# Optimization experiments

Hardware: AMD Instinct MI355X
Metric: run time of the kernel (lower is better)

The kernel has to match this reference:

```python
import jax, jax.numpy as jnp
import numpy as np

T = 2048          # num tokens (single long prefill sequence)
HID = 2048        # hidden_size
NH = 16           # num query heads
NKV = 2           # num kv heads
HD = 128          # head_dim (kv_channels)
ROPE_BASE = 10000.0


def setup_inputs() -> dict:
    key = jax.random.key(0)
    k1, k2, k3, k4, k5 = jax.random.split(key, 5)
    s = 0.02
    return {
        "hidden_states": jax.random.normal(k1, (T, HID), dtype=jnp.float32),
        "positions": jnp.arange(T, dtype=jnp.int64 if jax.config.jax_enable_x64 else jnp.int32),
        "Wq": jax.random.normal(k2, (NH * HD, HID), dtype=jnp.float32) * s,
        "Wk": jax.random.normal(k3, (NKV * HD, HID), dtype=jnp.float32) * s,
        "Wv": jax.random.normal(k4, (NKV * HD, HID), dtype=jnp.float32) * s,
        "Wo": jax.random.normal(k5, (HID, NH * HD), dtype=jnp.float32) * s,
    }


def _rope_cos_sin(positions):
    # fp32 RoPE tables, HF-style (concat of freqs with itself)
    inv_freq = 1.0 / (ROPE_BASE ** (jnp.arange(0, HD, 2, dtype=jnp.float32) / HD))
    freqs = positions.astype(jnp.float32)[:, None] * inv_freq[None, :]   # [T, HD/2]
    emb = jnp.concatenate([freqs, freqs], axis=-1)                        # [T, HD]
    return jnp.cos(emb)[:, None, :], jnp.sin(emb)[:, None, :]             # [T,1,HD]


def _rotate_half(x):
    x1, x2 = jnp.split(x, 2, axis=-1)
    return jnp.concatenate([-x2, x1], axis=-1)


def reference(hidden_states, positions, Wq, Wk, Wv, Wo):
    dtype = hidden_states.dtype
    # fused QKV projection (weights concatenated once, single GEMM)
    W_fused = jnp.concatenate([Wq, Wk, Wv], axis=0)            # [q+2kv, HID]
    qkv = hidden_states @ W_fused.T                             # [T, q+2kv]
    q, k, v = jnp.split(qkv, [NH * HD, NH * HD + NKV * HD], axis=-1)

    # fp32 RoPE on q/k
    cos, sin = _rope_cos_sin(positions)                         # [T,1,HD]
    qf = q.reshape(T, NH, HD).astype(jnp.float32)
    kf = k.reshape(T, NKV, HD).astype(jnp.float32)
    qf = qf * cos + _rotate_half(qf) * sin
    kf = kf * cos + _rotate_half(kf) * sin
    q = qf.astype(dtype)                                        # [T,NH,HD]
    k = kf.astype(dtype)                                        # [T,NKV,HD]
    v = v.reshape(T, NKV, HD)

    # causal GQA attention (same math as the paged-attention kernel on one seq)
    group = NH // NKV
    k_rep = jnp.repeat(k, group, axis=1)                        # [T,NH,HD]
    v_rep = jnp.repeat(v, group, axis=1)                        # [T,NH,HD]
    scale = HD ** -0.5
    scores = jnp.einsum('qhd,khd->hqk', q, k_rep) * scale       # [NH,T,T]
    causal = jnp.tril(jnp.ones((T, T), dtype=bool))
    scores = jnp.where(causal[None], scores, jnp.finfo(scores.dtype).min)
    probs = jax.nn.softmax(scores, axis=-1)
    attn = jnp.einsum('hqk,khd->qhd', probs, v_rep).reshape(T, NH * HD)

    return attn @ Wo.T                                          # [T, HID]
```

## Files before the change

### kernel.cpp

```cpp
#include <hip/hip_runtime.h>

#define T_TOK 2048
#define HID   2048
#define NH    16
#define NKV   2
#define HD    128
#define QDIM  (NH * HD)
#define KVDIM (NKV * HD)
#define QKVDIM (QDIM + 2 * KVDIM)

typedef float          f32x4  __attribute__((ext_vector_type(4)));
typedef unsigned short u16x8  __attribute__((ext_vector_type(8)));
typedef __bf16         bf16x8 __attribute__((ext_vector_type(8)));

__device__ __forceinline__ unsigned short f2bf(float f) {
    __bf16 h = (__bf16)f;
    return __builtin_bit_cast(unsigned short, h);
}
__device__ __forceinline__ float bf2f(unsigned short u) {
    return (float)__builtin_bit_cast(__bf16, u);
}

__device__ __forceinline__ f32x4 mfma16(u16x8 a, u16x8 b, f32x4 c) {
    return __builtin_amdgcn_mfma_f32_16x16x32_bf16(
        __builtin_bit_cast(bf16x8, a), __builtin_bit_cast(bf16x8, b), c, 0, 0, 0);
}

#define QSCL 0.12751743f
#define DEFER_THR 11.5416f

__global__ __launch_bounds__(256) void pack_bf16_all(
    const float* __restrict__ hidden, const float* __restrict__ Wq,
    const float* __restrict__ Wk, const float* __restrict__ Wv,
    const float* __restrict__ Wo,
    unsigned short* __restrict__ hb, unsigned short* __restrict__ Wf,
    unsigned short* __restrict__ Wob)
{
    const int b = blockIdx.x;
    const float* src; unsigned short* dst; size_t off;
    if      (b < 2048) { src = hidden; dst = hb;            off = (size_t)b * 2048; }
    else if (b < 4096) { src = Wq;     dst = Wf;            off = (size_t)(b - 2048) * 2048; }
    else if (b < 4352) { src = Wk;     dst = Wf + 4194304;  off = (size_t)(b - 4096) * 2048; }
    else if (b < 4608) { src = Wv;     dst = Wf + 4718592;  off = (size_t)(b - 4352) * 2048; }
    else               { src = Wo;     dst = Wob;           off = (size_t)(b - 4608) * 2048; }

    const size_t i = off + threadIdx.x * 8;
    float4 f0 = *reinterpret_cast<const float4*>(src + i);
    float4 f1 = *reinterpret_cast<const float4*>(src + i + 4);
    u16x8 o;
    o[0]=f2bf(f0.x); o[1]=f2bf(f0.y); o[2]=f2bf(f0.z); o[3]=f2bf(f0.w);
    o[4]=f2bf(f1.x); o[5]=f2bf(f1.y); o[6]=f2bf(f1.z); o[7]=f2bf(f1.w);
    *reinterpret_cast<u16x8*>(dst + i) = o;
}

template<bool BF16OUT>
__global__ __launch_bounds__(256) void gemm_bf16(
    const unsigned short* __restrict__ A,
    const unsigned short* __restrict__ B,
    void* __restrict__ Cv,
    int K, int NC, int nbx)
{
    __shared__ alignas(16) unsigned short As[2][128 * 64];
    __shared__ alignas(16) unsigned short Bs[2][128 * 64];

    const int tid  = threadIdx.x;
    const int lane = tid & 63;
    const int w    = tid >> 6;
    const int lg   = lane >> 4, lc = lane & 15;

    const int cpx = gridDim.x >> 3;
    const int wg  = (blockIdx.x & 7) * cpx + (blockIdx.x >> 3);
    const int m0  = (wg / nbx) * 128, n0 = (wg % nbx) * 128;

    const int rowL = lane >> 3;
    const int gS   = (lane & 7) ^ rowL;
    const int wr   = (w >> 1) * 64, wc = (w & 1) * 64;

    f32x4 acc[4][4] = {};

    auto stage = [&](int buf, int kb) {
        #pragma unroll
        for (int ci = 0; ci < 4; ci++) {
            const int chunk = w * 4 + ci;
            const int row   = chunk * 8 + rowL;
            const unsigned short* gpA = &A[(size_t)(m0 + row) * K + kb + gS * 8];
            __builtin_amdgcn_global_load_lds(
                (const __attribute__((address_space(1))) void*)gpA,
                (__attribute__((address_space(3))) void*)(&As[buf][chunk * 512]),
                16, 0, 0);
            const unsigned short* gpB = &B[(size_t)(n0 + row) * K + kb + gS * 8];
            __builtin_amdgcn_global_load_lds(
                (const __attribute__((address_space(1))) void*)gpB,
                (__attribute__((address_space(3))) void*)(&Bs[buf][chunk * 512]),
                16, 0, 0);
        }
    };

    stage(0, 0);
    const int nk = K >> 6;
    for (int t = 0; t < nk; ++t) {
        if (t + 1 < nk) {
            stage((t + 1) & 1, (t + 1) * 64);
            asm volatile("s_waitcnt vmcnt(8)" ::: "memory");
        } else {
            asm volatile("s_waitcnt vmcnt(0)" ::: "memory");
        }
        __syncthreads();

        const unsigned short* As_ = As[t & 1];
        const unsigned short* Bs_ = Bs[t & 1];
        #pragma unroll
        for (int kk = 0; kk < 2; kk++) {
            u16x8 af[4], bf[4];
            #pragma unroll
            for (int mi = 0; mi < 4; mi++) {
                const int r = wr + mi * 16 + lc;
                const int g = (kk * 4 + lg) ^ (lc & 7);
                af[mi] = *reinterpret_cast<const u16x8*>(&As_[r * 64 + g * 8]);
            }
            #pragma unroll
            for (int ni = 0; ni < 4; ni++) {
                const int r = wc + ni * 16 + lc;
                const int g = (kk * 4 + lg) ^ (lc & 7);
                bf[ni] = *reinterpret_cast<const u16x8*>(&Bs_[r * 64 + g * 8]);
            }
            #pragma unroll
            for (int mi = 0; mi < 4; mi++)
                #pragma unroll
                for (int ni = 0; ni < 4; ni++)
                    acc[mi][ni] = mfma16(af[mi], bf[ni], acc[mi][ni]);
        }
        __syncthreads();
    }

    #pragma unroll
    for (int mi = 0; mi < 4; mi++)
        #pragma unroll
        for (int ni = 0; ni < 4; ni++)
            #pragma unroll
            for (int j = 0; j < 4; j++) {
                const size_t idx = (size_t)(m0 + wr + mi * 16 + lg * 4 + j) * NC
                                   + n0 + wc + ni * 16 + lc;
                if constexpr (BF16OUT)
                    ((unsigned short*)Cv)[idx] = f2bf(acc[mi][ni][j]);
                else
                    ((float*)Cv)[idx] = acc[mi][ni][j];
            }
}

__global__ __launch_bounds__(256) void rope_kernel(
    const unsigned short* __restrict__ qkvb,
    const int* __restrict__ positions,
    unsigned short* __restrict__ qr,
    unsigned short* __restrict__ kr)
{
    const int t   = blockIdx.x;
    const int tid = threadIdx.x;
    __shared__ float cosv[64], sinv[64];

    if (tid < 64) {
        float invf = expf(-(float)tid * 0.14391156831212787f);
        float f = (float)positions[t] * invf;
        cosv[tid] = cosf(f);
        sinv[tid] = sinf(f);
    }
    __syncthreads();

    const unsigned short* row = qkvb + (size_t)t * QKVDIM;

    for (int i = tid; i < NH * 64; i += 256) {
        int hh = i >> 6, j = i & 63;
        float x1 = bf2f(row[hh * HD + j]);
        float x2 = bf2f(row[hh * HD + j + 64]);
        float c = cosv[j], s = sinv[j];
        qr[(size_t)t * QDIM + hh * HD + j]      = f2bf((x1 * c - x2 * s) * QSCL);
        qr[(size_t)t * QDIM + hh * HD + j + 64] = f2bf((x2 * c + x1 * s) * QSCL);
    }
    if (tid < NKV * 64) {
        int hh = tid >> 6, j = tid & 63;
        float x1 = bf2f(row[QDIM + hh * HD + j]);
        float x2 = bf2f(row[QDIM + hh * HD + j + 64]);
        float c = cosv[j], s = sinv[j];
        kr[(size_t)t * KVDIM + hh * HD + j]      = f2bf(x1 * c - x2 * s);
        kr[(size_t)t * KVDIM + hh * HD + j + 64] = f2bf(x2 * c + x1 * s);
    }
}

__global__ __launch_bounds__(256) void v_transpose(
    const unsigned short* __restrict__ qkvb,
    unsigned short* __restrict__ vt)
{
    __shared__ unsigned short tile[64][72];
    const int tid = threadIdx.x;
    const int t0  = blockIdx.x * 64;
    const int d0  = blockIdx.y * 64;

    {
        int r = tid >> 2;
        int c = (tid & 3) * 16;
        const unsigned short* src =
            &qkvb[(size_t)(t0 + r) * QKVDIM + QDIM + KVDIM + d0 + c];
        *reinterpret_cast<u16x8*>(&tile[r][c])     = *reinterpret_cast<const u16x8*>(src);
        *reinterpret_cast<u16x8*>(&tile[r][c + 8]) = *reinterpret_cast<const u16x8*>(src + 8);
    }
    __syncthreads();
    {
        int dr = tid >> 3;
        int tc = (tid & 7) * 8;
        #pragma unroll
        for (int i = 0; i < 2; i++) {
            int d = dr + i * 32;
            u16x8 ov;
            #pragma unroll
            for (int e = 0; e < 8; e++) ov[e] = tile[tc + e][d];
            *reinterpret_cast<u16x8*>(&vt[(size_t)(d0 + d) * T_TOK + t0 + tc]) = ov;
        }
    }
}

__global__ __launch_bounds__(256) void attn_kernel(
    const unsigned short* __restrict__ q,
    const unsigned short* __restrict__ k,
    const unsigned short* __restrict__ vt,
    unsigned short* __restrict__ o,
    float* __restrict__ pO,
    float* __restrict__ pML)
{
    __shared__ alignas(16) unsigned short Ks[2][64 * 128];
    __shared__ alignas(16) unsigned short Vs[2][128 * 64];
    __shared__ alignas(16) unsigned short P[4][16][72];

    const int tid  = threadIdx.x;
    const int lane = tid & 63;
    const int w    = tid >> 6;
    const int lg   = lane >> 4, lc = lane & 15;
    const int b    = blockIdx.x;
    const int h    = b & 15;
    const int idx  = b >> 4;

    int tau, c0;
    if (idx <= 16)      { tau = 15 + idx; c0 = 0; }
    else if (idx == 17) { tau = 31;       c0 = 1; }
    else {
        int j = idx - 18, kk = 15 - (j >> 1);
        if ((j & 1) == 0) { tau = kk - 1;  c0 = 0; }
        else              { tau = kk + 15; c0 = 1; }
    }
    const int kstart = c0 << 4;
    const int kcnt   = min(16, tau + 1 - kstart);

    const int q0   = tau * 64 + w * 16;
    const int hk   = h >> 3;
    const int xr   = (lc & 7) << 4;

    const int krow_l = (lane >> 4);
    const int kgS    = (lane & 15);
    const int vrow_l = (lane >> 3);
    const int vgS    = (lane & 7);

    u16x8 qf[4];
    #pragma unroll
    for (int dc = 0; dc < 4; dc++)
        qf[dc] = *reinterpret_cast<const u16x8*>(
            &q[(size_t)(q0 + lc) * QDIM + h * HD + dc * 32 + lg * 8]);

    float mrow = -1e30f, ell = 0.f;
    f32x4 oacc[8] = {};

    auto stage = [&](int buf, int kb) {
        #pragma unroll
        for (int ci = 0; ci < 4; ci++) {
            const int chunk = w * 4 + ci;
            const int row   = chunk * 4 + krow_l;
            const int gSk   = kgS ^ (row & 7);
            const unsigned short* gp =
                &k[(size_t)(kb + row) * KVDIM + hk * HD + gSk * 8];
            __builtin_amdgcn_global_load_lds(
                (const __attribute__((address_space(1))) void*)gp,
                (__attribute__((address_space(3))) void*)(&Ks[buf][chunk * 512]),
                16, 0, 0);
        }
        #pragma unroll
        for (int ci = 0; ci < 4; ci++) {
            const int chunk = w * 4 + ci;
            const int dr    = chunk * 8 + vrow_l;
            const int gSv   = vgS ^ (dr & 7);
            const unsigned short* gp =
                &vt[(size_t)(hk * HD + dr) * T_TOK + kb + gSv * 8];
            __builtin_amdgcn_global_load_lds(
                (const __attribute__((address_space(1))) void*)gp,
                (__attribute__((address_space(3))) void*)(&Vs[buf][chunk * 512]),
                16, 0, 0);
        }
    };

    stage(0, kstart * 64);
    for (int it = 0; it < kcnt; ++it) {
        if (it + 1 < kcnt) {
            stage((it + 1) & 1, (kstart + it + 1) * 64);
            asm volatile("s_waitcnt vmcnt(8)" ::: "memory");
        } else {
            asm volatile("s_waitcnt vmcnt(0)" ::: "memory");
        }
        __syncthreads();

        const int kb = (kstart + it) * 64;
        const char* KsB = (const char*)Ks[it & 1];
        const char* VsB = (const char*)Vs[it & 1];

        float sc[4][4];
        const bool dia = (kb + 63 > q0);
        #pragma unroll
        for (int c4 = 0; c4 < 4; c4++) {
            const int row = c4 * 16 + lc;
            f32x4 s = {0.f, 0.f, 0.f, 0.f};
            #pragma unroll
            for (int dc = 0; dc < 4; dc++) {
                u16x8 kf = *reinterpret_cast<const u16x8*>(
                    KsB + row * 256 + ((dc * 64 + lg * 16) ^ xr));
                s = mfma16(kf, qf[dc], s);
            }
            if (dia) {
                #pragma unroll
                for (int j = 0; j < 4; j++) {
                    const int kpos = kb + c4 * 16 + lg * 4 + j;
                    sc[c4][j] = (kpos <= q0 + lc) ? s[j] : -1e30f;
                }
            } else {
                #pragma unroll
                for (int j = 0; j < 4; j++) sc[c4][j] = s[j];
            }
        }

        float t01 = fmaxf(fmaxf(sc[0][0], sc[0][1]), fmaxf(sc[0][2], sc[0][3]));
        float t23 = fmaxf(fmaxf(sc[1][0], sc[1][1]), fmaxf(sc[1][2], sc[1][3]));
        float t45 = fmaxf(fmaxf(sc[2][0], sc[2][1]), fmaxf(sc[2][2], sc[2][3]));
        float t67 = fmaxf(fmaxf(sc[3][0], sc[3][1]), fmaxf(sc[3][2], sc[3][3]));
        float tmx = fmaxf(fmaxf(t01, t23), fmaxf(t45, t67));
        tmx = fmaxf(tmx, __shfl_xor(tmx, 16));
        tmx = fmaxf(tmx, __shfl_xor(tmx, 32));

        float mn;
        if (__all(tmx <= mrow + DEFER_THR)) {
            mn = mrow;
        } else {
            mn = fmaxf(mrow, tmx);
            float alpha = __builtin_amdgcn_exp2f(mrow - mn);
            mrow = mn;
            ell *= alpha;
            float aj[4];
            #pragma unroll
            for (int j = 0; j < 4; j++)
                aj[j] = __shfl(alpha, lg * 4 + j);
            #pragma unroll
            for (int d8 = 0; d8 < 8; d8++)
                #pragma unroll
                for (int j = 0; j < 4; j++)
                    oacc[d8][j] *= aj[j];
        }

        float rs = 0.f;
        #pragma unroll
        for (int c4 = 0; c4 < 4; c4++) {
            float p0 = __builtin_amdgcn_exp2f(sc[c4][0] - mn);
            float p1 = __builtin_amdgcn_exp2f(sc[c4][1] - mn);
            float p2 = __builtin_amdgcn_exp2f(sc[c4][2] - mn);
            float p3 = __builtin_amdgcn_exp2f(sc[c4][3] - mn);
            rs += (p0 + p1) + (p2 + p3);
            ushort4 pk;
            pk.x = f2bf(p0); pk.y = f2bf(p1); pk.z = f2bf(p2); pk.w = f2bf(p3);
            *reinterpret_cast<ushort4*>(&P[w][lc][c4 * 16 + lg * 4]) = pk;
        }
        rs += __shfl_xor(rs, 16);
        rs += __shfl_xor(rs, 32);
        ell += rs;

        asm volatile("s_waitcnt lgkmcnt(0)" ::: "memory");
        __builtin_amdgcn_sched_barrier(0);

        u16x8 pf0 = *reinterpret_cast<const u16x8*>(&P[w][lc][lg * 8]);
        u16x8 pf1 = *reinterpret_cast<const u16x8*>(&P[w][lc][32 + lg * 8]);

        #pragma unroll
        for (int d8 = 0; d8 < 8; d8++) {
            const int drow = d8 * 16 + lc;
            u16x8 vf0 = *reinterpret_cast<const u16x8*>(
                VsB + drow * 128 + ((lg * 16) ^ xr));
            u16x8 vf1 = *reinterpret_cast<const u16x8*>(
                VsB + drow * 128 + ((lg * 16 + 64) ^ xr));
            oacc[d8] = mfma16(pf0, vf0, oacc[d8]);
            oacc[d8] = mfma16(pf1, vf1, oacc[d8]);
        }
        __syncthreads();
    }

    if (tau < 16) {
        float ej[4];
        #pragma unroll
        for (int j = 0; j < 4; j++)
            ej[j] = __shfl(ell, lg * 4 + j);
        #pragma unroll
        for (int d8 = 0; d8 < 8; d8++)
            #pragma unroll
            for (int j = 0; j < 4; j++) {
                float val = oacc[d8][j] / ej[j];
                o[(size_t)(q0 + lg * 4 + j) * QDIM + h * HD + d8 * 16 + lc] = f2bf(val);
            }
    } else {
        const int s = (h * 16 + (tau - 16)) * 2 + c0;
        float* po = pO + (size_t)s * 8192;
        #pragma unroll
        for (int d8 = 0; d8 < 8; d8++)
            #pragma unroll
            for (int j = 0; j < 4; j++)
                po[(w * 16 + lg * 4 + j) * 128 + d8 * 16 + lc] = oacc[d8][j];
        if (lg == 0) {
            pML[s * 128 + w * 16 + lc]      = mrow;
            pML[s * 128 + 64 + w * 16 + lc] = ell;
        }
    }
}

__global__ __launch_bounds__(256) void attn_combine(
    const float* __restrict__ pO,
    const float* __restrict__ pML,
    unsigned short* __restrict__ o)
{
    const int b  = blockIdx.x;
    const int h  = b >> 4, ti = b & 15;
    const int tau = 16 + ti;
    const int s0 = (h * 16 + ti) * 2, s1 = s0 + 1;

    const int tid = threadIdx.x;
    const int r   = tid >> 2;
    const int cg  = (tid & 3) * 32;

    const float m1 = pML[s0 * 128 + r],      m2 = pML[s1 * 128 + r];
    const float l1 = pML[s0 * 128 + 64 + r], l2 = pML[s1 * 128 + 64 + r];
    const float M  = fmaxf(m1, m2);
    const float w1 = __builtin_amdgcn_exp2f(m1 - M);
    const float w2 = __builtin_amdgcn_exp2f(m2 - M);
    const float rn = 1.0f / (w1 * l1 + w2 * l2);

    const float* o1 = pO + (size_t)s0 * 8192 + r * 128 + cg;
    const float* o2 = pO + (size_t)s1 * 8192 + r * 128 + cg;
    unsigned short* dst = o + (size_t)(tau * 64 + r) * QDIM + h * HD + cg;

    #pragma unroll
    for (int i = 0; i < 8; i++) {
        float4 a = *reinterpret_cast<const float4*>(o1 + i * 4);
        float4 c = *reinterpret_cast<const float4*>(o2 + i * 4);
        ushort4 pk;
        pk.x = f2bf((w1 * a.x + w2 * c.x) * rn);
        pk.y = f2bf((w1 * a.y + w2 * c.y) * rn);
        pk.z = f2bf((w1 * a.z + w2 * c.z) * rn);
        pk.w = f2bf((w1 * a.w + w2 * c.w) * rn);
        *reinterpret_cast<ushort4*>(dst + i * 4) = pk;
    }
}

extern "C" void kernel_launch(void* const* d_in, const int* in_sizes, int n_in,
                              void* d_out, int out_size, void* d_ws, size_t ws_size,
                              hipStream_t stream) {
    const float* hidden    = (const float*)d_in[0];
    const int*   positions = (const int*)d_in[1];
    const float* Wq        = (const float*)d_in[2];
    const float* Wk        = (const float*)d_in[3];
    const float* Wv        = (const float*)d_in[4];
    const float* Wo        = (const float*)d_in[5];
    float*       out       = (float*)d_out;

    char* ws = (char*)d_ws;
    unsigned short* qkvb = (unsigned short*)(ws);
    unsigned short* qr  = (unsigned short*)(ws + 20971520);
    unsigned short* kr  = (unsigned short*)(ws + 29360128);
    unsigned short* vt  = (unsigned short*)(ws + 30408704);
    unsigned short* att = (unsigned short*)(ws + 31457280);
    unsigned short* hb  = (unsigned short*)(ws + 39845888);
    unsigned short* Wf  = (unsigned short*)(ws + 48234496);
    unsigned short* Wob = (unsigned short*)(ws + 58720256);
    float* pO  = (float*)(ws);
    float* pML = (float*)(ws + 16777216);

    pack_bf16_all<<<6656, 256, 0, stream>>>(hidden, Wq, Wk, Wv, Wo, hb, Wf, Wob);
    gemm_bf16<true><<<320, 256, 0, stream>>>(hb, Wf, qkvb, HID, QKVDIM, QKVDIM / 128);
    rope_kernel<<<T_TOK, 256, 0, stream>>>(qkvb, positions, qr, kr);
    v_transpose<<<dim3(T_TOK / 64, KVDIM / 64), 256, 0, stream>>>(qkvb, vt);
    attn_kernel<<<NH * 48, 256, 0, stream>>>(qr, kr, vt, att, pO, pML);
    attn_combine<<<256, 256, 0, stream>>>(pO, pML, att);
    gemm_bf16<false><<<256, 256, 0, stream>>>(att, Wob, out, QDIM, HID, HID / 128);
}
```

Measured before the change: 145.6 us.

## Split attention into 8-tile KV chunks with table schedule, fuse rope and V transpose

Attention work is now split into chunks of at most 8 KV tiles, so long query tiles get up to 4 partial blocks. The blocks are ordered by a static schedule table, 1280 blocks instead of 768, with a combine kernel that merges up to 4 partials. The double-buffered K/V staging is replaced by single-buffered LDS, which halves shared memory per block and should let more blocks reside on each CU. The RoPE and V-transpose kernels are merged into one launch to save a kernel launch. In exchange, loads no longer overlap compute within a block, and the extra partial writes and combine reads add memory traffic.

```diff
diff --git a/kernel.cpp b/kernel.cpp
--- a/kernel.cpp
+++ b/kernel.cpp
@@ -28,6 +28,29 @@
 
 #define QSCL 0.12751743f
 #define DEFER_THR 11.5416f
+
+__device__ __forceinline__ float* slotO(char* b, int s) {
+    return (float*)(s < 640 ? b + (size_t)s * 32768
+                            : b + 39845888 + (size_t)(s - 640) * 32768);
+}
+#define PML_OFF 56623104
+
+__device__ const unsigned char SCH_TAU[80] = {
+ 31,31,31,31, 30,30,30, 29,29,29, 28,28,28, 27,27,27, 26,26,26, 25,25,25, 24,24,24, 23,23,23,
+ 22,22, 21,21, 20,20, 19,19, 18,18, 17,17, 16,16, 15,15,
+ 14,13,12,11,10,9,8,7,
+ 30,22,14,6, 29,21,13,5, 28,20,12,4, 27,19,11,3, 26,18,10,2, 25,17,9,1, 24,16,8,0 };
+__device__ const unsigned char SCH_C[80] = {
+ 0,1,2,3, 0,1,2, 0,1,2, 0,1,2, 0,1,2, 0,1,2, 0,1,2, 0,1,2, 0,1,2,
+ 0,1, 0,1, 0,1, 0,1, 0,1, 0,1, 0,1, 0,1,
+ 0,0,0,0,0,0,0,0,
+ 3,2,1,0, 3,2,1,0, 3,2,1,0, 3,2,1,0, 3,2,1,0, 3,2,1,0, 3,2,1,0 };
+
+__device__ __forceinline__ int tile_local(int tau) {
+    return tau < 16 ? (tau - 8) * 2
+         : tau < 24 ? 16 + (tau - 16) * 3
+                    : 40 + (tau - 24) * 4;
+}
 
 __global__ __launch_bounds__(256) void pack_bf16_all(
     const float* __restrict__ hidden, const float* __restrict__ Wq,
@@ -148,72 +171,68 @@
             }
 }
 
-__global__ __launch_bounds__(256) void rope_kernel(
+__global__ __launch_bounds__(256) void rope_vt(
     const unsigned short* __restrict__ qkvb,
     const int* __restrict__ positions,
     unsigned short* __restrict__ qr,
-    unsigned short* __restrict__ kr)
-{
-    const int t   = blockIdx.x;
-    const int tid = threadIdx.x;
-    __shared__ float cosv[64], sinv[64];
-
-    if (tid < 64) {
-        float invf = expf(-(float)tid * 0.14391156831212787f);
-        float f = (float)positions[t] * invf;
-        cosv[tid] = cosf(f);
-        sinv[tid] = sinf(f);
-    }
-    __syncthreads();
-
-    const unsigned short* row = qkvb + (size_t)t * QKVDIM;
-
-    for (int i = tid; i < NH * 64; i += 256) {
-        int hh = i >> 6, j = i & 63;
-        float x1 = bf2f(row[hh * HD + j]);
-        float x2 = bf2f(row[hh * HD + j + 64]);
-        float c = cosv[j], s = sinv[j];
-        qr[(size_t)t * QDIM + hh * HD + j]      = f2bf((x1 * c - x2 * s) * QSCL);
-        qr[(size_t)t * QDIM + hh * HD + j + 64] = f2bf((x2 * c + x1 * s) * QSCL);
-    }
-    if (tid < NKV * 64) {
-        int hh = tid >> 6, j = tid & 63;
-        float x1 = bf2f(row[QDIM + hh * HD + j]);
-        float x2 = bf2f(row[QDIM + hh * HD + j + 64]);
-        float c = cosv[j], s = sinv[j];
-        kr[(size_t)t * KVDIM + hh * HD + j]      = f2bf(x1 * c - x2 * s);
-        kr[(size_t)t * KVDIM + hh * HD + j + 64] = f2bf(x2 * c + x1 * s);
-    }
-}
-
-__global__ __launch_bounds__(256) void v_transpose(
-    const unsigned short* __restrict__ qkvb,
+    unsigned short* __restrict__ kr,
     unsigned short* __restrict__ vt)
 {
+    __shared__ float cosv[64], sinv[64];
     __shared__ unsigned short tile[64][72];
     const int tid = threadIdx.x;
-    const int t0  = blockIdx.x * 64;
-    const int d0  = blockIdx.y * 64;
-
-    {
-        int r = tid >> 2;
-        int c = (tid & 3) * 16;
-        const unsigned short* src =
-            &qkvb[(size_t)(t0 + r) * QKVDIM + QDIM + KVDIM + d0 + c];
-        *reinterpret_cast<u16x8*>(&tile[r][c])     = *reinterpret_cast<const u16x8*>(src);
-        *reinterpret_cast<u16x8*>(&tile[r][c + 8]) = *reinterpret_cast<const u16x8*>(src + 8);
-    }
-    __syncthreads();
-    {
-        int dr = tid >> 3;
-        int tc = (tid & 7) * 8;
-        #pragma unroll
-        for (int i = 0; i < 2; i++) {
-            int d = dr + i * 32;
-            u16x8 ov;
-            #pragma unroll
-            for (int e = 0; e < 8; e++) ov[e] = tile[tc + e][d];
-            *reinterpret_cast<u16x8*>(&vt[(size_t)(d0 + d) * T_TOK + t0 + tc]) = ov;
+
+    if (blockIdx.x < 2048) {
+        const int t = blockIdx.x;
+        if (tid < 64) {
+            float invf = expf(-(float)tid * 0.14391156831212787f);
+            float f = (float)positions[t] * invf;
+            cosv[tid] = cosf(f);
+            sinv[tid] = sinf(f);
+        }
+        __syncthreads();
+
+        const unsigned short* row = qkvb + (size_t)t * QKVDIM;
+        for (int i = tid; i < NH * 64; i += 256) {
+            int hh = i >> 6, j = i & 63;
+            float x1 = bf2f(row[hh * HD + j]);
+            float x2 = bf2f(row[hh * HD + j + 64]);
+            float c = cosv[j], s = sinv[j];
+            qr[(size_t)t * QDIM + hh * HD + j]      = f2bf((x1 * c - x2 * s) * QSCL);
+            qr[(size_t)t * QDIM + hh * HD + j + 64] = f2bf((x2 * c + x1 * s) * QSCL);
+        }
+        if (tid < NKV * 64) {
+            int hh = tid >> 6, j = tid & 63;
+            float x1 = bf2f(row[QDIM + hh * HD + j]);
+            float x2 = bf2f(row[QDIM + hh * HD + j + 64]);
+            float c = cosv[j], s = sinv[j];
+            kr[(size_t)t * KVDIM + hh * HD + j]      = f2bf(x1 * c - x2 * s);
+            kr[(size_t)t * KVDIM + hh * HD + j + 64] = f2bf(x2 * c + x1 * s);
+        }
+    } else {
+        const int bb = blockIdx.x - 2048;
+        const int t0 = (bb & 31) * 64;
+        const int d0 = (bb >> 5) * 64;
+        {
+            int r = tid >> 2;
+            int c = (tid & 3) * 16;
+            const unsigned short* src =
+                &qkvb[(size_t)(t0 + r) * QKVDIM + QDIM + KVDIM + d0 + c];
+            *reinterpret_cast<u16x8*>(&tile[r][c])     = *reinterpret_cast<const u16x8*>(src);
+            *reinterpret_cast<u16x8*>(&tile[r][c + 8]) = *reinterpret_cast<const u16x8*>(src + 8);
+        }
+        __syncthreads();
+        {
+            int dr = tid >> 3;
+            int tc = (tid & 7) * 8;
+            #pragma unroll
+            for (int i = 0; i < 2; i++) {
+                int d = dr + i * 32;
+                u16x8 ov;
+                #pragma unroll
+                for (int e = 0; e < 8; e++) ov[e] = tile[tc + e][d];
+                *reinterpret_cast<u16x8*>(&vt[(size_t)(d0 + d) * T_TOK + t0 + tc]) = ov;
+            }
         }
     }
 }
@@ -223,11 +242,10 @@
     const unsigned short* __restrict__ k,
     const unsigned short* __restrict__ vt,
     unsigned short* __restrict__ o,
-    float* __restrict__ pO,
-    float* __restrict__ pML)
+    char* __restrict__ wsb)
 {
-    __shared__ alignas(16) unsigned short Ks[2][64 * 128];
-    __shared__ alignas(16) unsigned short Vs[2][128 * 64];
+    __shared__ alignas(16) unsigned short Ks[64 * 128];
+    __shared__ alignas(16) unsigned short Vs[128 * 64];
     __shared__ alignas(16) unsigned short P[4][16][72];
 
     const int tid  = threadIdx.x;
@@ -236,18 +254,12 @@
     const int lg   = lane >> 4, lc = lane & 15;
     const int b    = blockIdx.x;
     const int h    = b & 15;
-    const int idx  = b >> 4;
-
-    int tau, c0;
-    if (idx <= 16)      { tau = 15 + idx; c0 = 0; }
-    else if (idx == 17) { tau = 31;       c0 = 1; }
-    else {
-        int j = idx - 18, kk = 15 - (j >> 1);
-        if ((j & 1) == 0) { tau = kk - 1;  c0 = 0; }
-        else              { tau = kk + 15; c0 = 1; }
-    }
-    const int kstart = c0 << 4;
-    const int kcnt   = min(16, tau + 1 - kstart);
+    const int e    = b >> 4;
+
+    const int tau  = SCH_TAU[e];
+    const int c0   = SCH_C[e];
+    const int kstart = c0 * 8;
+    const int kcnt   = min(8, tau + 1 - kstart);
 
     const int q0   = tau * 64 + w * 16;
     const int hk   = h >> 3;
@@ -267,7 +279,7 @@
     float mrow = -1e30f, ell = 0.f;
     f32x4 oacc[8] = {};
 
-    auto stage = [&](int buf, int kb) {
+    auto stage = [&](int kb) {
         #pragma unroll
         for (int ci = 0; ci < 4; ci++) {
             const int chunk = w * 4 + ci;
@@ -277,7 +289,7 @@
                 &k[(size_t)(kb + row) * KVDIM + hk * HD + gSk * 8];
             __builtin_amdgcn_global_load_lds(
                 (const __attribute__((address_space(1))) void*)gp,
-                (__attribute__((address_space(3))) void*)(&Ks[buf][chunk * 512]),
+                (__attribute__((address_space(3))) void*)(&Ks[chunk * 512]),
                 16, 0, 0);
         }
         #pragma unroll
@@ -289,24 +301,19 @@
                 &vt[(size_t)(hk * HD + dr) * T_TOK + kb + gSv * 8];
             __builtin_amdgcn_global_load_lds(
                 (const __attribute__((address_space(1))) void*)gp,
-                (__attribute__((address_space(3))) void*)(&Vs[buf][chunk * 512]),
+                (__attribute__((address_space(3))) void*)(&Vs[chunk * 512]),
                 16, 0, 0);
         }
     };
 
-    stage(0, kstart * 64);
     for (int it = 0; it < kcnt; ++it) {
-        if (it + 1 < kcnt) {
-            stage((it + 1) & 1, (kstart + it + 1) * 64);
-            asm volatile("s_waitcnt vmcnt(8)" ::: "memory");
-        } else {
-            asm volatile("s_waitcnt vmcnt(0)" ::: "memory");
-        }
+        const int kb = (kstart + it) * 64;
+        stage(kb);
+        asm volatile("s_waitcnt vmcnt(4)" ::: "memory");
         __syncthreads();
 
-        const int kb = (kstart + it) * 64;
-        const char* KsB = (const char*)Ks[it & 1];
-        const char* VsB = (const char*)Vs[it & 1];
+        const char* KsB = (const char*)Ks;
+        const char* VsB = (const char*)Vs;
 
         float sc[4][4];
         const bool dia = (kb + 63 > q0);
@@ -375,8 +382,9 @@
         rs += __shfl_xor(rs, 32);
         ell += rs;
 
-        asm volatile("s_waitcnt lgkmcnt(0)" ::: "memory");
+        asm volatile("s_waitcnt vmcnt(0) lgkmcnt(0)" ::: "memory");
         __builtin_amdgcn_sched_barrier(0);
+        __syncthreads();
 
         u16x8 pf0 = *reinterpret_cast<const u16x8*>(&P[w][lc][lg * 8]);
         u16x8 pf1 = *reinterpret_cast<const u16x8*>(&P[w][lc][32 + lg * 8]);
@@ -391,10 +399,10 @@
             oacc[d8] = mfma16(pf0, vf0, oacc[d8]);
             oacc[d8] = mfma16(pf1, vf1, oacc[d8]);
         }
-        __syncthreads();
+        if (it + 1 < kcnt) __syncthreads();
     }
 
-    if (tau < 16) {
+    if (tau <= 7) {
         float ej[4];
         #pragma unroll
         for (int j = 0; j < 4; j++)
@@ -407,55 +415,75 @@
                 o[(size_t)(q0 + lg * 4 + j) * QDIM + h * HD + d8 * 16 + lc] = f2bf(val);
             }
     } else {
-        const int s = (h * 16 + (tau - 16)) * 2 + c0;
-        float* po = pO + (size_t)s * 8192;
+        const int slot = h * 72 + tile_local(tau) + c0;
+        float* po = slotO(wsb, slot);
+        float* pML = (float*)(wsb + PML_OFF);
         #pragma unroll
         for (int d8 = 0; d8 < 8; d8++)
             #pragma unroll
             for (int j = 0; j < 4; j++)
                 po[(w * 16 + lg * 4 + j) * 128 + d8 * 16 + lc] = oacc[d8][j];
         if (lg == 0) {
-            pML[s * 128 + w * 16 + lc]      = mrow;
-            pML[s * 128 + 64 + w * 16 + lc] = ell;
+            pML[slot * 128 + w * 16 + lc]      = mrow;
+            pML[slot * 128 + 64 + w * 16 + lc] = ell;
         }
     }
 }
 
 __global__ __launch_bounds__(256) void attn_combine(
-    const float* __restrict__ pO,
-    const float* __restrict__ pML,
+    char* __restrict__ wsb,
     unsigned short* __restrict__ o)
 {
-    const int b  = blockIdx.x;
-    const int h  = b >> 4, ti = b & 15;
-    const int tau = 16 + ti;
-    const int s0 = (h * 16 + ti) * 2, s1 = s0 + 1;
+    const int ti  = blockIdx.x;
+    const int h   = blockIdx.y;
+    const int tau = 8 + ti;
+    const int nch = (tau + 8) >> 3;
+    const int sb  = h * 72 + tile_local(tau);
+    const float* pML = (const float*)(wsb + PML_OFF);
 
     const int tid = threadIdx.x;
     const int r   = tid >> 2;
     const int cg  = (tid & 3) * 32;
 
-    const float m1 = pML[s0 * 128 + r],      m2 = pML[s1 * 128 + r];
-    const float l1 = pML[s0 * 128 + 64 + r], l2 = pML[s1 * 128 + 64 + r];
-    const float M  = fmaxf(m1, m2);
-    const float w1 = __builtin_amdgcn_exp2f(m1 - M);
-    const float w2 = __builtin_amdgcn_exp2f(m2 - M);
-    const float rn = 1.0f / (w1 * l1 + w2 * l2);
-
-    const float* o1 = pO + (size_t)s0 * 8192 + r * 128 + cg;
-    const float* o2 = pO + (size_t)s1 * 8192 + r * 128 + cg;
+    float m0v = pML[(sb + 0) * 128 + r], l0v = pML[(sb + 0) * 128 + 64 + r];
+    float m1v = pML[(sb + 1) * 128 + r], l1v = pML[(sb + 1) * 128 + 64 + r];
+    float m2v = -1e30f, l2v = 0.f, m3v = -1e30f, l3v = 0.f;
+    if (nch > 2) { m2v = pML[(sb + 2) * 128 + r]; l2v = pML[(sb + 2) * 128 + 64 + r]; }
+    if (nch > 3) { m3v = pML[(sb + 3) * 128 + r]; l3v = pML[(sb + 3) * 128 + 64 + r]; }
+
+    const float M  = fmaxf(fmaxf(m0v, m1v), fmaxf(m2v, m3v));
+    const float w0 = __builtin_amdgcn_exp2f(m0v - M);
+    const float w1 = __builtin_amdgcn_exp2f(m1v - M);
+    const float w2 = nch > 2 ? __builtin_amdgcn_exp2f(m2v - M) : 0.f;
+    const float w3 = nch > 3 ? __builtin_amdgcn_exp2f(m3v - M) : 0.f;
+    const float rn = 1.0f / (w0 * l0v + w1 * l1v + w2 * l2v + w3 * l3v);
+
+    const float* o0 = slotO(wsb, sb + 0) + r * 128 + cg;
+    const float* o1 = slotO(wsb, sb + 1) + r * 128 + cg;
+    const float* o2 = slotO(wsb, sb + 2) + r * 128 + cg;
+    const float* o3 = slotO(wsb, sb + 3) + r * 128 + cg;
     unsigned short* dst = o + (size_t)(tau * 64 + r) * QDIM + h * HD + cg;
 
     #pragma unroll
-    for (int i = 0; i < 8; i++) {
-        float4 a = *reinterpret_cast<const float4*>(o1 + i * 4);
-        float4 c = *reinterpret_cast<const float4*>(o2 + i * 4);
+    for (int g = 0; g < 8; g++) {
+        float4 a0 = *reinterpret_cast<const float4*>(o0 + g * 4);
+        float4 a1 = *reinterpret_cast<const float4*>(o1 + g * 4);
+        float ax = w0 * a0.x + w1 * a1.x;
+        float ay = w0 * a0.y + w1 * a1.y;
+        float az = w0 * a0.z + w1 * a1.z;
+        float aw = w0 * a0.w + w1 * a1.w;
+        if (nch > 2) {
+            float4 a2 = *reinterpret_cast<const float4*>(o2 + g * 4);
+            ax += w2 * a2.x; ay += w2 * a2.y; az += w2 * a2.z; aw += w2 * a2.w;
+        }
+        if (nch > 3) {
+            float4 a3 = *reinterpret_cast<const float4*>(o3 + g * 4);
+            ax += w3 * a3.x; ay += w3 * a3.y; az += w3 * a3.z; aw += w3 * a3.w;
+        }
         ushort4 pk;
-        pk.x = f2bf((w1 * a.x + w2 * c.x) * rn);
-        pk.y = f2bf((w1 * a.y + w2 * c.y) * rn);
-        pk.z = f2bf((w1 * a.z + w2 * c.z) * rn);
-        pk.w = f2bf((w1 * a.w + w2 * c.w) * rn);
-        *reinterpret_cast<ushort4*>(dst + i * 4) = pk;
+        pk.x = f2bf(ax * rn); pk.y = f2bf(ay * rn);
+        pk.z = f2bf(az * rn); pk.w = f2bf(aw * rn);
+        *reinterpret_cast<ushort4*>(dst + g * 4) = pk;
     }
 }
 
@@ -479,14 +507,11 @@
     unsigned short* hb  = (unsigned short*)(ws + 39845888);
     unsigned short* Wf  = (unsigned short*)(ws + 48234496);
     unsigned short* Wob = (unsigned short*)(ws + 58720256);
-    float* pO  = (float*)(ws);
-    float* pML = (float*)(ws + 16777216);
 
     pack_bf16_all<<<6656, 256, 0, stream>>>(hidden, Wq, Wk, Wv, Wo, hb, Wf, Wob);
     gemm_bf16<true><<<320, 256, 0, stream>>>(hb, Wf, qkvb, HID, QKVDIM, QKVDIM / 128);
-    rope_kernel<<<T_TOK, 256, 0, stream>>>(qkvb, positions, qr, kr);
-    v_transpose<<<dim3(T_TOK / 64, KVDIM / 64), 256, 0, stream>>>(qkvb, vt);
-    attn_kernel<<<NH * 48, 256, 0, stream>>>(qr, kr, vt, att, pO, pML);
-    attn_combine<<<256, 256, 0, stream>>>(pO, pML, att);
+    rope_vt<<<2176, 256, 0, stream>>>(qkvb, positions, qr, kr, vt);
+    attn_kernel<<<1280, 256, 0, stream>>>(qr, kr, vt, att, ws);
+    attn_combine<<<dim3(24, 16), 256, 0, stream>>>(ws, att);
     gemm_bf16<false><<<256, 256, 0, stream>>>(att, Wob, out, QDIM, HID, HID / 128);
 }
```

Result: slower. 158.1 us (+8.6%).
